# Performance work log

Measured on AMD Instinct MI355X. Metric: run time of the kernel, lower is better.

The kernel has to match this reference:

```python
import jax, jax.numpy as jnp
import numpy as np

H = W = 32
C = 512
RED = 16


def make_gus(v=1.5):
    # gus[p=(i,k), x, y] = exp(-((x-i)^2+(y-k)^2)/(2 v^2)) / (2 pi v^2), normalized per p.
    idx = np.arange(H, dtype=np.float64)
    d2 = (idx[:, None] - idx[None, :]) ** 2          # [center, coord]
    g1 = np.exp(-d2 / (2.0 * v * v))                  # separable factor
    g = np.einsum('ix,ky->ikxy', g1, g1) / (2.0 * np.pi * v * v)
    g = g / g.sum(axis=(2, 3), keepdims=True)         # per-position normalization
    return jnp.asarray(g.reshape(H * W, H, W), dtype=jnp.float32)


def setup_inputs() -> dict:
    key = jax.random.key(0)
    ks = jax.random.split(key, 6)
    b = 16
    return {
        'x': jax.random.normal(ks[0], (b, C, H, W), dtype=jnp.float32),
        'se_w1': jax.random.normal(ks[1], (C // RED, C), dtype=jnp.float32) * 0.02,
        'se_b1': jnp.zeros((C // RED,), dtype=jnp.float32),
        'se_w2': jax.random.normal(ks[2], (C, C // RED), dtype=jnp.float32) * 0.02,
        'se_b2': jnp.zeros((C,), dtype=jnp.float32),
        'down_w': jax.random.normal(ks[3], (C, 2 * C), dtype=jnp.float32) * 0.02,
        'gus': make_gus(1.5),
    }


def _patches3(img, h, w):
    # img: [b, c, h+2, w+2] -> [b, c, h, w, 9] (3x3 neighborhoods, row-major dy*3+dx)
    ps = [img[:, :, dy:dy + h, dx:dx + w] for dy in range(3) for dx in range(3)]
    return jnp.stack(ps, axis=-1)


def reference(x, se_w1, se_b1, se_w2, se_b2, down_w, gus):
    b, c, h, w = x.shape
    # --- SELayer ---
    s = x.mean(axis=(2, 3))                                   # [b, c]
    y = jax.nn.relu(s @ se_w1.T + se_b1)                       # [b, c/16]
    y = jax.nn.sigmoid(y @ se_w2.T + se_b2)                    # [b, c]
    out32 = x * y[:, :, None, None]
    # --- gaussian-weighted global pooling per output position ---
    # g[b, p, ch] = sum_{y,x} gus[p,y,x] * out32[b,ch,y,x]; then torch's view(c,h,w)
    gus_out = jnp.einsum('pyx,bcyx->bpc', gus, out32).reshape(b, c, h, w)
    # --- patch self-attention ---
    sig = jax.nn.sigmoid(out32)
    sigp = _patches3(jnp.pad(sig, ((0, 0), (0, 0), (1, 1), (1, 1))), h, w)    # [b,c,h,w,9]
    ffp = _patches3(jnp.pad(out32, ((0, 0), (0, 0), (1, 1), (1, 1))), h, w)   # [b,c,h,w,9]
    logits = jnp.einsum('bcyx,bcyxk->byxk', sig, sigp) / c     # mean over channels
    attn = jax.nn.softmax(logits, axis=-1)                     # softmax over 3x3 patch
    g2 = jnp.einsum('byxk,bcyxk->byxc', attn, ffp)             # [b,h,w,c] = [b, p, c]
    out_csa = g2.reshape(b, c, h, w)                           # torch view(c,h,w) of [hw,c]
    # --- down: 1x1 conv (no bias) + InstanceNorm2d + LeakyReLU(0.2) ---
    cat = jnp.concatenate([gus_out, out_csa], axis=1)          # [b, 2c, h, w]
    z = jnp.einsum('oi,biyx->boyx', down_w, cat)
    mu = z.mean(axis=(2, 3), keepdims=True)
    var = z.var(axis=(2, 3), keepdims=True)
    zn = (z - mu) * jax.lax.rsqrt(var + 1e-5)
    return jnp.where(zn >= 0, zn, 0.2 * zn)
```

## Files before the change

### kernel.cpp

```cpp
#include <hip/hip_runtime.h>
#include <stdint.h>

#define NB 16
#define NC 512
#define NS 1024
#define NR 32

typedef unsigned short u16;
typedef unsigned int u32;

typedef __attribute__((ext_vector_type(8))) short short8;
typedef __attribute__((ext_vector_type(4))) float f32x4;

__device__ __forceinline__ float bf2f(u16 u) {
    union { u32 i; float f; } c; c.i = ((u32)u) << 16; return c.f;
}
__device__ __forceinline__ u16 f2bf(float f) {
    union { float f; u32 i; } c; c.f = f;
    u32 r = (c.i + 0x7FFFu + ((c.i >> 16) & 1u)) >> 16;
    return (u16)r;
}
__device__ __forceinline__ float sigm(float x) {
    return 1.0f / (1.0f + __expf(-x));
}

#define GLD16(gp, lp)                                                      \
    __builtin_amdgcn_global_load_lds(                                      \
        (const __attribute__((address_space(1))) u32*)(gp),                \
        (__attribute__((address_space(3))) u32*)(lp), 16, 0, 0)

__global__ void k_pre(const float* __restrict__ x, float* __restrict__ sm,
                      const float* __restrict__ dw, u16* __restrict__ dwb,
                      const float* __restrict__ g, u16* __restrict__ gt) {
    __shared__ __align__(16) float shb[64 * 65];
    const int t = threadIdx.x;
    if (blockIdx.x < NB * NC) {
        const int row = blockIdx.x;
        const float4* xr = (const float4*)(x + (long)row * NS);
        float4 v = xr[t];
        float p = v.x + v.y + v.z + v.w;
        for (int off = 32; off; off >>= 1) p += __shfl_down(p, off);
        if ((t & 63) == 0) shb[t >> 6] = p;
        __syncthreads();
        if (t == 0) sm[row] = (shb[0] + shb[1] + shb[2] + shb[3]) * (1.0f / 1024.0f);
    } else if (blockIdx.x < NB * NC + 2048) {
        const int i = (blockIdx.x - NB * NC) * 256 + t;
        dwb[i] = f2bf(dw[i]);
    } else {
        const int gbx = blockIdx.x - (NB * NC + 2048);
        const int p0 = (gbx & 15) * 64;
        const int k0 = (gbx >> 4) * 64;
        float (*tile)[65] = (float(*)[65])shb;
#pragma unroll
        for (int it = 0; it < 4; ++it) {
            int c = it * 256 + t;
            int row = c >> 4;
            int f4 = c & 15;
            float4 v = *(const float4*)&g[(long)(p0 + row) * 1024 + k0 + f4 * 4];
            tile[row][f4 * 4 + 0] = v.x; tile[row][f4 * 4 + 1] = v.y;
            tile[row][f4 * 4 + 2] = v.z; tile[row][f4 * 4 + 3] = v.w;
        }
        __syncthreads();
        const int q = t >> 7, k_loc = t & 63, h = (t >> 6) & 1;
        short8 v0, v1;
#pragma unroll
        for (int jj = 0; jj < 8; ++jj) {
            v0[jj] = (short)f2bf(tile[2 * (h * 16 + jj) + q][k_loc]);
            v1[jj] = (short)f2bf(tile[2 * (h * 16 + 8 + jj) + q][k_loc]);
        }
        long ob = (long)q * 524288 + (long)(k0 + k_loc) * 512 + (p0 >> 1) + h * 16;
        *(short8*)&gt[ob] = v0;
        *(short8*)&gt[ob + 8] = v1;
    }
}

#define MFMA_TILE_STEP(As, Bs)                                                      \
    {                                                                               \
        _Pragma("unroll")                                                           \
        for (int kk = 0; kk < 128; kk += 32) {                                      \
            const int gq = (kk >> 3) + (lane >> 4);                                 \
            const int slot = gq ^ (lane & 15);                                      \
            short8 af[4], bfr[4];                                                   \
            _Pragma("unroll")                                                       \
            for (int i = 0; i < 4; ++i)                                             \
                af[i] = *(const short8*)&As[(wm + i * 16 + (lane & 15)) * 128 + slot * 8]; \
            _Pragma("unroll")                                                       \
            for (int j = 0; j < 4; ++j)                                             \
                bfr[j] = *(const short8*)&Bs[(wn + j * 16 + (lane & 15)) * 128 + slot * 8]; \
            _Pragma("unroll")                                                       \
            for (int i = 0; i < 4; ++i)                                             \
                _Pragma("unroll")                                                   \
                for (int j = 0; j < 4; ++j)                                         \
                    acc[i][j] = __builtin_amdgcn_mfma_f32_16x16x32_bf16(af[i], bfr[j], acc[i][j], 0, 0, 0); \
        }                                                                           \
    }

__global__ __launch_bounds__(256)
void k_we(const u16* __restrict__ dwb, const u16* __restrict__ gt,
          u16* __restrict__ Eb, const float* __restrict__ sm,
          const float* __restrict__ w1, const float* __restrict__ b1,
          const float* __restrict__ w2, const float* __restrict__ b2,
          float* __restrict__ y) {
    __shared__ __align__(16) u16 As[128 * 128];
    __shared__ __align__(16) u16 Bs[128 * 128];
    const int bx = blockIdx.x;
    const int tid = threadIdx.x;
    if (bx < 64) {
        const int q = bx >> 5, rem = bx & 31;
        const int m0 = (rem >> 3) * 128, n0 = (rem & 7) * 128;
        const u16* Bb = gt + (long)q * 524288;
        const int lane = tid & 63, wave = tid >> 6;
        const int wm = (wave >> 1) * 64, wn = (wave & 1) * 64;
        f32x4 acc[4][4];
#pragma unroll
        for (int i = 0; i < 4; ++i)
#pragma unroll
            for (int j = 0; j < 4; ++j) acc[i][j] = (f32x4){0.f, 0.f, 0.f, 0.f};
        int srow[8], sg8[8];
#pragma unroll
        for (int r = 0; r < 8; ++r) {
            int c = r * 256 + tid;
            srow[r] = c >> 4;
            sg8[r] = ((c & 15) ^ (srow[r] & 15)) * 8;
        }
        for (int k0 = 0; k0 < 512; k0 += 128) {
#pragma unroll
            for (int r = 0; r < 8; ++r) {
                const int c = r * 256 + tid;
                GLD16(dwb + (long)(m0 + srow[r]) * 1024 + (k0 + sg8[r]), &As[c * 8]);
                GLD16(Bb + (long)(n0 + srow[r]) * 512 + (k0 + sg8[r]), &Bs[c * 8]);
            }
            __syncthreads();
            MFMA_TILE_STEP(As, Bs);
            __syncthreads();
        }
        const int col = lane & 15, rq = (lane >> 4) * 4;
#pragma unroll
        for (int i = 0; i < 4; ++i)
#pragma unroll
            for (int j = 0; j < 4; ++j)
#pragma unroll
                for (int r = 0; r < 4; ++r) {
                    int row = m0 + wm + i * 16 + rq + r;
                    int ncol = n0 + wn + j * 16 + col;
                    Eb[(long)q * 524288 + (long)row * 1024 + ncol] = f2bf(acc[i][j][r]);
                }
    } else {
        const int b = bx - 64;
        float* s_s = (float*)As;
        float* s_y1 = (float*)Bs;
        const int t = tid;
        s_s[t] = sm[b * NC + t];
        s_s[t + 256] = sm[b * NC + t + 256];
        __syncthreads();
        {
            const int r = t >> 3, sub = t & 7;
            const float4* wr = (const float4*)(w1 + r * NC + sub * 64);
            const float4* sv = (const float4*)(s_s + sub * 64);
            float acc = 0.f;
#pragma unroll
            for (int i = 0; i < 16; ++i) {
                float4 wv = wr[i];
                float4 s4 = sv[i];
                acc += wv.x * s4.x + wv.y * s4.y + wv.z * s4.z + wv.w * s4.w;
            }
            acc += __shfl_down(acc, 4);
            acc += __shfl_down(acc, 2);
            acc += __shfl_down(acc, 1);
            if (sub == 0) s_y1[r] = fmaxf(acc + b1[r], 0.0f);
        }
        __syncthreads();
        for (int i = 0; i < 2; ++i) {
            int c = t + i * 256;
            float acc = b2[c];
#pragma unroll
            for (int r = 0; r < NR; ++r) acc += s_y1[r] * w2[c * NR + r];
            y[b * NC + c] = 1.0f / (1.0f + expf(-acc));
        }
    }
}

__global__ void k_scale(const float* __restrict__ x, const float* __restrict__ y,
                        u16* __restrict__ o32, u16* __restrict__ o32t) {
    const int b = blockIdx.z;
    const int c0 = blockIdx.y * 32;
    const int s0 = blockIdx.x * 32;
    const int tx = threadIdx.x & 31, ty = threadIdx.x >> 5;
    __shared__ float tile[32][33];
    const float* xb = x + (long)b * NC * NS;
#pragma unroll
    for (int it = 0; it < 4; ++it) {
        int c = c0 + ty + it * 8;
        float v = xb[(long)c * NS + s0 + tx] * y[b * NC + c];
        tile[ty + it * 8][tx] = v;
        o32[((long)b * NC + c) * NS + s0 + tx] = f2bf(v);
    }
    __syncthreads();
#pragma unroll
    for (int it = 0; it < 4; ++it) {
        int sr = ty + it * 8;
        float tv = tile[tx][sr];
        long idx = ((long)b * NS + (s0 + sr)) * NC + c0 + tx;
        o32t[idx] = f2bf(tv);
    }
}

__global__ __launch_bounds__(256)
void k_attn(const u16* __restrict__ o32t, u16* __restrict__ g2) {
    const int wave = threadIdx.x >> 6, lane = threadIdx.x & 63;
    const int tid = threadIdx.x;
    const int bx = blockIdx.x;
    const int b = blockIdx.y;
    const int y0 = bx >> 3;
    const int xbase = (bx & 7) * 4;
    const long base = (long)b * NS * NC;
    __shared__ __align__(16) u16 smem[2 * 18 * NC];

#pragma unroll
    for (int r = 0; r < 5; ++r) {
        int idx = r * 256 + tid;
        if (idx < 18 * 64) {
            int pair = idx >> 6;
            int ch0 = (idx & 63) * 8;
            int yy = y0 + pair / 6 - 1;
            int xx = xbase + pair % 6 - 1;
            short8 v = (short8){0, 0, 0, 0, 0, 0, 0, 0};
            short8 sv = (short8){0, 0, 0, 0, 0, 0, 0, 0};
            if (yy >= 0 && yy < 32 && xx >= 0 && xx < 32) {
                v = *(const short8*)&o32t[base + (long)(yy * 32 + xx) * NC + ch0];
#pragma unroll
                for (int j = 0; j < 8; ++j) sv[j] = (short)f2bf(sigm(bf2f((u16)v[j])));
            }
            *(short8*)&smem[(18 + pair) * NC + ch0] = v;
            *(short8*)&smem[pair * NC + ch0] = sv;
        }
    }
    __syncthreads();

    const int coff = lane * 8;
    short8 csv = *(const short8*)&smem[(6 + wave + 1) * NC + coff];
    float sc[8];
#pragma unroll
    for (int j = 0; j < 8; ++j) sc[j] = bf2f((u16)csv[j]);

    float part[9];
#pragma unroll
    for (int k = 0; k < 9; ++k) {
        int pair = (k / 3) * 6 + wave + k % 3;
        short8 sv = *(const short8*)&smem[pair * NC + coff];
        float p = 0.f;
#pragma unroll
        for (int j = 0; j < 8; ++j) p += sc[j] * bf2f((u16)sv[j]);
        part[k] = p;
    }
#pragma unroll
    for (int k = 0; k < 9; ++k)
        for (int off = 32; off; off >>= 1) part[k] += __shfl_down(part[k], off);

    if (lane == 0) {
        float mx = -1e30f;
#pragma unroll
        for (int k = 0; k < 9; ++k) { part[k] *= (1.0f / 512.0f); mx = fmaxf(mx, part[k]); }
        float sum = 0.f;
#pragma unroll
        for (int k = 0; k < 9; ++k) { part[k] = __expf(part[k] - mx); sum += part[k]; }
        float inv = 1.0f / sum;
#pragma unroll
        for (int k = 0; k < 9; ++k) part[k] *= inv;
    }
    float g[8] = {0.f, 0.f, 0.f, 0.f, 0.f, 0.f, 0.f, 0.f};
#pragma unroll
    for (int k = 0; k < 9; ++k) {
        float a = __shfl(part[k], 0);
        int pair = (k / 3) * 6 + wave + k % 3;
        short8 rv = *(const short8*)&smem[(18 + pair) * NC + coff];
#pragma unroll
        for (int j = 0; j < 8; ++j) g[j] += a * bf2f((u16)rv[j]);
    }
    short8 ov;
#pragma unroll
    for (int j = 0; j < 8; ++j) ov[j] = (short)f2bf(g[j]);
    const int s = y0 * 32 + xbase + wave;
    *(short8*)&g2[base + (long)s * NC + coff] = ov;
}

__global__ __launch_bounds__(256)
void k_tr2(const u16* __restrict__ g2, u16* __restrict__ gs) {
    const int b = blockIdx.y;
    const int c0 = (blockIdx.x & 7) * 64;
    const int j0 = ((blockIdx.x >> 3) & 7) * 64;
    const int q = blockIdx.x >> 6;
    const int t = threadIdx.x;
    __shared__ __align__(16) u16 tile[64 * 64];
    const u16* src = g2 + (long)b * 524288 + (long)(2 * j0 + q) * 512 + c0;
#pragma unroll
    for (int it = 0; it < 2; ++it) {
        int c = it * 256 + t;
        int jl = c >> 3, sg = c & 7;
        short8 v = *(const short8*)&src[(long)jl * 1024 + sg * 8];
        int slot = sg ^ ((jl >> 3) & 7);
        *(short8*)&tile[jl * 64 + slot * 8] = v;
    }
    __syncthreads();
#pragma unroll
    for (int it = 0; it < 2; ++it) {
        int c = it * 256 + t;
        int cl = c >> 3, jg = c & 7;
        const int gcs = cl >> 3, co = cl & 7;
        short8 v;
#pragma unroll
        for (int jj = 0; jj < 8; ++jj) {
            int j = jg * 8 + jj;
            int slot = gcs ^ jg;
            v[jj] = (short)tile[j * 64 + slot * 8 + co];
        }
        *(short8*)&gs[(long)b * 524288 + (long)q * 262144 +
                      (long)(c0 + cl) * 512 + j0 + jg * 8] = v;
    }
}

__global__ __launch_bounds__(256)
void k_zgemm(const u16* __restrict__ Em, const u16* __restrict__ dwb,
             const u16* __restrict__ o32, const u16* __restrict__ gsep,
             u16* __restrict__ Z) {
    const int b = blockIdx.z;
    const int band = blockIdx.y & 1;
    const int m0 = (blockIdx.y >> 1) * 128;
    const int n0 = blockIdx.x * 128;
    __shared__ __align__(16) u16 As[128 * 128];
    __shared__ __align__(16) u16 Bs[128 * 128];
    const int tid = threadIdx.x;
    const int lane = tid & 63, wave = tid >> 6;
    const int wm = (wave >> 1) * 64, wn = (wave & 1) * 64;
    f32x4 acc[4][4];
#pragma unroll
    for (int i = 0; i < 4; ++i)
#pragma unroll
        for (int j = 0; j < 4; ++j) acc[i][j] = (f32x4){0.f, 0.f, 0.f, 0.f};

    int srow[8], sg8[8];
#pragma unroll
    for (int r = 0; r < 8; ++r) {
        int c = r * 256 + tid;
        srow[r] = c >> 4;
        sg8[r] = ((c & 15) ^ (srow[r] & 15)) * 8;
    }
    const u16* A0 = Em + (long)band * 524288;
    const u16* B0 = o32 + (long)b * 524288;
    const u16* A1 = dwb + 512;
    const u16* B1 = gsep + (long)b * 524288 + (long)band * 262144;

    for (int k0 = 0; k0 < 1024; k0 += 128) {
#pragma unroll
        for (int r = 0; r < 8; ++r) {
            const int c = r * 256 + tid;
            GLD16(A0 + (long)(m0 + srow[r]) * 1024 + (k0 + sg8[r]), &As[c * 8]);
            GLD16(B0 + (long)(n0 + srow[r]) * 1024 + (k0 + sg8[r]), &Bs[c * 8]);
        }
        __syncthreads();
        MFMA_TILE_STEP(As, Bs);
        __syncthreads();
    }
    for (int k0 = 0; k0 < 512; k0 += 128) {
#pragma unroll
        for (int r = 0; r < 8; ++r) {
            const int c = r * 256 + tid;
            GLD16(A1 + (long)(m0 + srow[r]) * 1024 + (k0 + sg8[r]), &As[c * 8]);
            GLD16(B1 + (long)(n0 + srow[r]) * 512 + (k0 + sg8[r]), &Bs[c * 8]);
        }
        __syncthreads();
        MFMA_TILE_STEP(As, Bs);
        __syncthreads();
    }
    const int col = lane & 15, rq = (lane >> 4) * 4;
#pragma unroll
    for (int i = 0; i < 4; ++i)
#pragma unroll
        for (int j = 0; j < 4; ++j)
#pragma unroll
            for (int r = 0; r < 4; ++r) {
                int row = m0 + wm + i * 16 + rq + r;
                int ncol = n0 + wn + j * 16 + col;
                Z[((long)b * 512 + row) * 1024 + band * 512 + ncol] = f2bf(acc[i][j][r]);
            }
}

__global__ void k_norm(const u16* __restrict__ z, float* __restrict__ out) {
    const int row = blockIdx.x;
    const int t = threadIdx.x;
    uint2 u = ((const uint2*)(z + (long)row * NS))[t];
    float v0 = bf2f((u16)(u.x & 0xffffu)), v1 = bf2f((u16)(u.x >> 16));
    float v2 = bf2f((u16)(u.y & 0xffffu)), v3 = bf2f((u16)(u.y >> 16));
    float sm = v0 + v1 + v2 + v3;
    float sq = v0 * v0 + v1 * v1 + v2 * v2 + v3 * v3;
    for (int off = 32; off; off >>= 1) { sm += __shfl_down(sm, off); sq += __shfl_down(sq, off); }
    __shared__ __align__(16) float rs[4], rq2[4];
    if ((t & 63) == 0) { rs[t >> 6] = sm; rq2[t >> 6] = sq; }
    __syncthreads();
    float tot = rs[0] + rs[1] + rs[2] + rs[3];
    float totq = rq2[0] + rq2[1] + rq2[2] + rq2[3];
    float mu = tot * (1.0f / 1024.0f);
    float var = totq * (1.0f / 1024.0f) - mu * mu;
    float sc = rsqrtf(var + 1e-5f);
    float4 o;
    float a;
    a = (v0 - mu) * sc; o.x = (a >= 0.f) ? a : 0.2f * a;
    a = (v1 - mu) * sc; o.y = (a >= 0.f) ? a : 0.2f * a;
    a = (v2 - mu) * sc; o.z = (a >= 0.f) ? a : 0.2f * a;
    a = (v3 - mu) * sc; o.w = (a >= 0.f) ? a : 0.2f * a;
    ((float4*)(out + (long)row * NS))[t] = o;
}

extern "C" void kernel_launch(void* const* d_in, const int* in_sizes, int n_in,
                              void* d_out, int out_size, void* d_ws, size_t ws_size,
                              hipStream_t stream) {
    const float* x   = (const float*)d_in[0];
    const float* w1  = (const float*)d_in[1];
    const float* b1  = (const float*)d_in[2];
    const float* w2  = (const float*)d_in[3];
    const float* b2  = (const float*)d_in[4];
    const float* dw  = (const float*)d_in[5];
    const float* gus = (const float*)d_in[6];
    float* out = (float*)d_out;
    char* ws = (char*)d_ws;

    float* sm_buf = (float*)(ws + 0);
    float* y_buf  = (float*)(ws + 32768);
    u16* dwbf     = (u16*)(ws + 65536);
    u16* gusTb    = (u16*)(ws + 1114112);
    u16* Ebuf     = (u16*)(ws + 3211264);
    u16* o32      = (u16*)(ws + 5308416);
    u16* o32t     = (u16*)(ws + 22085632);
    u16* g2b      = (u16*)(ws + 38862848);
    u16* g2sep    = (u16*)(ws + 22085632);
    u16* Z        = (u16*)(ws + 38862848);

    k_pre<<<dim3(NB * NC + 2048 + 256), dim3(256), 0, stream>>>(
        x, sm_buf, dw, dwbf, gus, gusTb);
    k_we<<<dim3(80), dim3(256), 0, stream>>>(
        dwbf, gusTb, Ebuf, sm_buf, w1, b1, w2, b2, y_buf);
    k_scale<<<dim3(32, 16, NB), dim3(256), 0, stream>>>(x, y_buf, o32, o32t);
    k_attn<<<dim3(256, NB), dim3(256), 0, stream>>>(o32t, g2b);
    k_tr2<<<dim3(128, NB), dim3(256), 0, stream>>>(g2b, g2sep);
    k_zgemm<<<dim3(4, 8, NB), dim3(256), 0, stream>>>(Ebuf, dwbf, o32, g2sep, Z);
    k_norm<<<dim3(NB * NC), dim3(256), 0, stream>>>(Z, out);
}
```

Baseline: 193.4 us.

## Widen attention tiles to 8 pixels and precompute sigmoid in scale kernel

The attention kernel now handles 8 output pixels per block with 512 threads and a 3x10 halo, where it used 4 pixels and a 3x6 halo. This cuts redundant halo loads per output. When the workspace is large enough, k_scale also writes a transposed bf16 sigmoid buffer, so the attention kernel loads it instead of recomputing sigmoid over the halo. The cost is an extra 16MB write in k_scale and an extra read in k_attn, and it needs a larger workspace; otherwise the on-the-fly path is used.

```diff
diff --git a/kernel.cpp b/kernel.cpp
--- a/kernel.cpp
+++ b/kernel.cpp
@@ -181,7 +181,8 @@
 }
 
 __global__ void k_scale(const float* __restrict__ x, const float* __restrict__ y,
-                        u16* __restrict__ o32, u16* __restrict__ o32t) {
+                        u16* __restrict__ o32, u16* __restrict__ o32t,
+                        u16* __restrict__ sig_t) {
     const int b = blockIdx.z;
     const int c0 = blockIdx.y * 32;
     const int s0 = blockIdx.x * 32;
@@ -202,43 +203,53 @@
         float tv = tile[tx][sr];
         long idx = ((long)b * NS + (s0 + sr)) * NC + c0 + tx;
         o32t[idx] = f2bf(tv);
-    }
-}
-
-__global__ __launch_bounds__(256)
-void k_attn(const u16* __restrict__ o32t, u16* __restrict__ g2) {
+        if (sig_t) sig_t[idx] = f2bf(sigm(tv));
+    }
+}
+
+template <bool ONFLY>
+__global__ __launch_bounds__(512)
+void k_attn(const u16* __restrict__ sig_t, const u16* __restrict__ o32t,
+            u16* __restrict__ g2) {
     const int wave = threadIdx.x >> 6, lane = threadIdx.x & 63;
     const int tid = threadIdx.x;
     const int bx = blockIdx.x;
     const int b = blockIdx.y;
-    const int y0 = bx >> 3;
-    const int xbase = (bx & 7) * 4;
+    const int y0 = bx >> 2;
+    const int xbase = (bx & 3) * 8;
     const long base = (long)b * NS * NC;
-    __shared__ __align__(16) u16 smem[2 * 18 * NC];
-
-#pragma unroll
-    for (int r = 0; r < 5; ++r) {
-        int idx = r * 256 + tid;
-        if (idx < 18 * 64) {
+    __shared__ __align__(16) u16 smem[2 * 30 * NC];
+
+#pragma unroll
+    for (int it = 0; it < 4; ++it) {
+        int idx = it * 512 + tid;
+        if (idx < 30 * 64) {
             int pair = idx >> 6;
             int ch0 = (idx & 63) * 8;
-            int yy = y0 + pair / 6 - 1;
-            int xx = xbase + pair % 6 - 1;
-            short8 v = (short8){0, 0, 0, 0, 0, 0, 0, 0};
+            int prow = pair / 10;
+            int pxc = pair - prow * 10;
+            int yy = y0 + prow - 1;
+            int xx = xbase + pxc - 1;
+            short8 rv = (short8){0, 0, 0, 0, 0, 0, 0, 0};
             short8 sv = (short8){0, 0, 0, 0, 0, 0, 0, 0};
             if (yy >= 0 && yy < 32 && xx >= 0 && xx < 32) {
-                v = *(const short8*)&o32t[base + (long)(yy * 32 + xx) * NC + ch0];
-#pragma unroll
-                for (int j = 0; j < 8; ++j) sv[j] = (short)f2bf(sigm(bf2f((u16)v[j])));
+                long roff = base + (long)(yy * 32 + xx) * NC + ch0;
+                rv = *(const short8*)&o32t[roff];
+                if (ONFLY) {
+#pragma unroll
+                    for (int j = 0; j < 8; ++j) sv[j] = (short)f2bf(sigm(bf2f((u16)rv[j])));
+                } else {
+                    sv = *(const short8*)&sig_t[roff];
+                }
             }
-            *(short8*)&smem[(18 + pair) * NC + ch0] = v;
             *(short8*)&smem[pair * NC + ch0] = sv;
+            *(short8*)&smem[(30 + pair) * NC + ch0] = rv;
         }
     }
     __syncthreads();
 
     const int coff = lane * 8;
-    short8 csv = *(const short8*)&smem[(6 + wave + 1) * NC + coff];
+    short8 csv = *(const short8*)&smem[(11 + wave) * NC + coff];
     float sc[8];
 #pragma unroll
     for (int j = 0; j < 8; ++j) sc[j] = bf2f((u16)csv[j]);
@@ -246,7 +257,7 @@
     float part[9];
 #pragma unroll
     for (int k = 0; k < 9; ++k) {
-        int pair = (k / 3) * 6 + wave + k % 3;
+        int pair = (k / 3) * 10 + wave + k % 3;
         short8 sv = *(const short8*)&smem[pair * NC + coff];
         float p = 0.f;
 #pragma unroll
@@ -272,8 +283,8 @@
 #pragma unroll
     for (int k = 0; k < 9; ++k) {
         float a = __shfl(part[k], 0);
-        int pair = (k / 3) * 6 + wave + k % 3;
-        short8 rv = *(const short8*)&smem[(18 + pair) * NC + coff];
+        int pair = (k / 3) * 10 + wave + k % 3;
+        short8 rv = *(const short8*)&smem[(30 + pair) * NC + coff];
 #pragma unroll
         for (int j = 0; j < 8; ++j) g[j] += a * bf2f((u16)rv[j]);
     }
@@ -431,16 +442,21 @@
     u16* Ebuf     = (u16*)(ws + 3211264);
     u16* o32      = (u16*)(ws + 5308416);
     u16* o32t     = (u16*)(ws + 22085632);
-    u16* g2b      = (u16*)(ws + 38862848);
+    const bool big = (ws_size >= 72417280UL);
+    u16* sig_t    = big ? (u16*)(ws + 38862848) : (u16*)0;
+    u16* g2b      = big ? (u16*)(ws + 55640064) : (u16*)(ws + 38862848);
     u16* g2sep    = (u16*)(ws + 22085632);
-    u16* Z        = (u16*)(ws + 38862848);
+    u16* Z        = g2b;
 
     k_pre<<<dim3(NB * NC + 2048 + 256), dim3(256), 0, stream>>>(
         x, sm_buf, dw, dwbf, gus, gusTb);
     k_we<<<dim3(80), dim3(256), 0, stream>>>(
         dwbf, gusTb, Ebuf, sm_buf, w1, b1, w2, b2, y_buf);
-    k_scale<<<dim3(32, 16, NB), dim3(256), 0, stream>>>(x, y_buf, o32, o32t);
-    k_attn<<<dim3(256, NB), dim3(256), 0, stream>>>(o32t, g2b);
+    k_scale<<<dim3(32, 16, NB), dim3(256), 0, stream>>>(x, y_buf, o32, o32t, sig_t);
+    if (big)
+        k_attn<false><<<dim3(128, NB), dim3(512), 0, stream>>>(sig_t, o32t, g2b);
+    else
+        k_attn<true><<<dim3(128, NB), dim3(512), 0, stream>>>(sig_t, o32t, g2b);
     k_tr2<<<dim3(128, NB), dim3(256), 0, stream>>>(g2b, g2sep);
     k_zgemm<<<dim3(4, 8, NB), dim3(256), 0, stream>>>(Ebuf, dwbf, o32, g2sep, Z);
     k_norm<<<dim3(NB * NC), dim3(256), 0, stream>>>(Z, out);
```

New measurement: 186.0 us. 1.04x faster.
